# Performance work log

Hardware: AMD Instinct MI355X
Metric: run time of the kernel (lower is better)

Reference implementation:

```python
import jax, jax.numpy as jnp
import numpy as np

D, P, MC = 512, 256, 128   # state dim, obs dim, control dim
H, M, T = 32, 64, 1024     # num filters, Hankel/filter length, horizon
GAMMA = 0.9


def setup_inputs() -> dict:
    rng = np.random.default_rng(0)
    # Stable dynamics: scale spectral radius to 0.95
    A = rng.standard_normal((D, D)).astype(np.float32)
    A *= np.float32(0.95 / np.max(np.abs(np.linalg.eigvals(A))))
    B = (rng.standard_normal((D, MC)) / np.sqrt(D)).astype(np.float32)
    C = (rng.standard_normal((P, D)) / np.sqrt(D)).astype(np.float32)
    # SPD cost matrices
    Q_obs = np.eye(P, dtype=np.float32)
    R = (0.1 * np.eye(MC)).astype(np.float32)
    # LQR-like feedback gain (small, applied to y_obs as in the source)
    K = (0.02 * rng.standard_normal((MC, P))).astype(np.float32)
    # Spectral filters from Hankel matrix: Z_ij = gamma^(i+j+2) * 2/((i+j+2)^3-(i+j+2))
    idx = np.arange(M)
    ij = idx[:, None] + idx[None, :] + 2
    Z = (GAMMA ** ij) * 2.0 / (ij ** 3 - ij)
    w, V = np.linalg.eigh(Z)
    sigma = np.abs(w[-H:])
    phi = V[:, -H:]
    sigma_phi = (sigma ** 0.25)[:, None] * phi.T        # [H, M]
    sigma_phi_M = sigma_phi.astype(np.float32)
    # sum over the inner l-loop of sigma_phi_m (the source sums contributions over l)
    s_m = sigma_phi.sum(axis=1).astype(np.float32)       # [H]
    # Learned controller tensor M_il -> [m_control, H, h, p]
    M_tensor = (0.01 * rng.standard_normal((MC, H, H, P))).astype(np.float32)
    x0 = rng.standard_normal(D).astype(np.float32)
    return {
        "A": jnp.asarray(A), "B": jnp.asarray(B), "C": jnp.asarray(C),
        "Q_obs": jnp.asarray(Q_obs), "R": jnp.asarray(R), "K": jnp.asarray(K),
        "M_tensor": jnp.asarray(M_tensor),
        "sigma_phi_M": jnp.asarray(sigma_phi_M), "s_m": jnp.asarray(s_m),
        "x0": jnp.asarray(x0),
    }


def reference(A, B, C, Q_obs, R, K, M_tensor, sigma_phi_M, s_m, x0):
    h, m = sigma_phi_M.shape          # filters, history window
    mc = B.shape[1]
    p = C.shape[0]

    # CAB[i] = C @ A^i @ B for i = 0..h  (Markov parameters for y_nat)
    def pow_step(Ap, _):
        return Ap @ A, C @ (Ap @ B)
    _, CAB = jax.lax.scan(pow_step, jnp.eye(A.shape[0], dtype=A.dtype), None, length=h + 1)  # [h+1, p, mc]

    # Pre-contract M_tensor with the inner filter weights (sum over j/l):
    # u_pert[c] = sum_{i,k,p'} M2[c,i,p'] * sigma_phi_M[i,k] * y_nat_{t-k}[p']
    M2 = jnp.einsum('cijq,j->ciq', M_tensor, s_m)  # [mc, h, p]

    def step(carry, _):
        x, u_buf, y_buf = carry            # x:[d], u_buf:[h+1,mc] newest-first, y_buf:[m,p] newest-first
        y_obs = C @ x                      # [p]
        # natural observation: strip effect of past controls
        y_nat = y_obs - jnp.einsum('ipc,ic->p', CAB, u_buf)
        y_buf = jnp.concatenate([y_nat[None, :], y_buf[:-1]], axis=0)
        # spectral projection of y_nat history, then contract with learned tensor
        y_proj = sigma_phi_M @ y_buf       # [h, p]
        u_pert = jnp.einsum('ciq,iq->c', M2, y_proj)  # [mc]
        u = -(K @ y_obs) + u_pert
        cost = y_obs @ (Q_obs @ y_obs) + u @ (R @ u)
        u_buf = jnp.concatenate([u[None, :], u_buf[:-1]], axis=0)
        x = A @ x + B @ u
        return (x, u_buf, y_buf), cost

    init = (x0,
            jnp.zeros((h + 1, mc), dtype=x0.dtype),
            jnp.zeros((m, p), dtype=x0.dtype))
    _, costs = jax.lax.scan(step, init, None, length=T)
    return costs  # [T] per-step losses
```

## Files before the change

### kernel.cpp

```cpp
#include <hip/hip_runtime.h>

#define TPB 256
#define MAXJ 48

#define SC_N 128
#define YD0 128
#define YU0 160
#define WD0 167
#define WU0 175
#define DT0 182
#define XP0 198
#define XR0 230
#define U0 246
#define NWG 254
#define NGRP 8
#define GCH 32

__device__ __forceinline__ void cst(float* p, float v) {
  __hip_atomic_store(p, v, __ATOMIC_RELAXED, __HIP_MEMORY_SCOPE_AGENT);
}
__device__ __forceinline__ void cstu(unsigned* p, unsigned v) {
  __hip_atomic_store(p, v, __ATOMIC_RELAXED, __HIP_MEMORY_SCOPE_AGENT);
}
__device__ __forceinline__ unsigned cldu(const unsigned* p) {
  return __hip_atomic_load(p, __ATOMIC_RELAXED, __HIP_MEMORY_SCOPE_AGENT);
}
__device__ __forceinline__ float cld(const float* p) {
  return __hip_atomic_load(p, __ATOMIC_RELAXED, __HIP_MEMORY_SCOPE_AGENT);
}
__device__ __forceinline__ float2 cld2(const float* p) {
  unsigned long long u = __hip_atomic_load(
      reinterpret_cast<const unsigned long long*>(p), __ATOMIC_RELAXED,
      __HIP_MEMORY_SCOPE_AGENT);
  float2 v;
  __builtin_memcpy(&v, &u, 8);
  return v;
}

__device__ __forceinline__ void grid_barrier(unsigned* __restrict__ arr,
                                             unsigned* __restrict__ grp,
                                             int bid, int tid, unsigned phase) {
  asm volatile("s_waitcnt vmcnt(0)" ::: "memory");
  __syncthreads();
  if (tid == 0) cstu(arr + (bid << 5), phase);
  if (bid < NGRP) {
    const int lo = bid * GCH;
    const int n = (NWG - lo < GCH) ? (NWG - lo) : GCH;
    if (tid < n) {
      while (cldu(arr + ((lo + tid) << 5)) < phase) __builtin_amdgcn_s_sleep(1);
    }
    __syncthreads();
    if (tid == 0) cstu(grp + (bid << 5), phase);
  }
  if (tid < NGRP) {
    while (cldu(grp + (tid << 5)) < phase) __builtin_amdgcn_s_sleep(1);
  }
  __atomic_signal_fence(__ATOMIC_SEQ_CST);
  __syncthreads();
}

__device__ void gemm_tile(const float* __restrict__ X, const float* __restrict__ Y,
                          float* __restrict__ Z, int M, int N, int Kd,
                          int mtile, int ntile) {
  __shared__ float Xs[16][65];
  __shared__ float Ys[16][65];
  const int tx = threadIdx.x & 15;
  const int ty = threadIdx.x >> 4;
  const int mbase = mtile * 64;
  const int nbase = ntile * 64;
  float acc[4][4] = {};
  for (int k0 = 0; k0 < Kd; k0 += 16) {
#pragma unroll
    for (int r = 0; r < 4; ++r) {
      int idx = threadIdx.x + 256 * r;
      int mm = idx >> 4, kk = idx & 15;
      int gm = mbase + mm, gk = k0 + kk;
      Xs[kk][mm] = (gm < M && gk < Kd) ? X[(size_t)gm * Kd + gk] : 0.f;
      int nn = idx & 63, k2 = idx >> 6;
      int gn = nbase + nn, gk2 = k0 + k2;
      Ys[k2][nn] = (gk2 < Kd && gn < N) ? Y[(size_t)gk2 * N + gn] : 0.f;
    }
    __syncthreads();
#pragma unroll
    for (int kk = 0; kk < 16; ++kk) {
      float xv[4], yv[4];
#pragma unroll
      for (int a = 0; a < 4; ++a) xv[a] = Xs[kk][ty * 4 + a];
#pragma unroll
      for (int b = 0; b < 4; ++b) yv[b] = Ys[kk][tx * 4 + b];
#pragma unroll
      for (int a = 0; a < 4; ++a)
#pragma unroll
        for (int b = 0; b < 4; ++b) acc[a][b] += xv[a] * yv[b];
    }
    __syncthreads();
  }
#pragma unroll
  for (int a = 0; a < 4; ++a) {
    int gm = mbase + ty * 4 + a;
    if (gm < M) {
#pragma unroll
      for (int b = 0; b < 4; ++b) {
        int gn = nbase + tx * 4 + b;
        if (gn < N) Z[(size_t)gm * N + gn] = acc[a][b];
      }
    }
  }
}

struct JobBatch {
  int n;
  int start[MAXJ + 1];
  int xsel[MAXJ], xoff[MAXJ], ysel[MAXJ], yoff[MAXJ], zoff[MAXJ];
  int M[MAXJ], N[MAXJ], K[MAXJ];
};

__global__ __launch_bounds__(256) void multi_gemm(JobBatch jb,
    const float* __restrict__ A, const float* __restrict__ Bm,
    const float* __restrict__ C, const float* __restrict__ Km,
    float* __restrict__ ws) {
  int b = blockIdx.x;
  int j = 0;
  while (j < jb.n - 1 && b >= jb.start[j + 1]) ++j;
  int rel = b - jb.start[j];
  const float* bases[5] = {ws, A, Bm, C, Km};
  const float* X = bases[jb.xsel[j]] + jb.xoff[j];
  const float* Y = bases[jb.ysel[j]] + jb.yoff[j];
  float* Z = ws + jb.zoff[j];
  int tn = jb.N[j] >> 6;
  gemm_tile(X, Y, Z, jb.M[j], jb.N[j], jb.K[j], rel / tn, rel % tn);
}

__global__ __launch_bounds__(256) void m2_kernel(const float* __restrict__ MT,
    const float* __restrict__ sm, float* __restrict__ M2g) {
  int idx = blockIdx.x * 256 + threadIdx.x;
  if (idx >= 128 * 32 * 256) return;
  int q = idx & 255;
  int ci = idx >> 8;
  const float* base = MT + (size_t)ci * 32 * 256 + q;
  float acc = 0.f;
#pragma unroll
  for (int j = 0; j < 32; ++j) acc += base[j * 256] * sm[j];
  M2g[idx] = acc;
}

__global__ __launch_bounds__(256) void wfir_kernel(const float* __restrict__ M2g,
    const float* __restrict__ Phi, float* __restrict__ W) {
  int idx = blockIdx.x * 256 + threadIdx.x;
  if (idx >= 64 * 32768) return;
  int j = idx >> 15;
  int cq = idx & 32767;
  int c = cq >> 8;
  int q = cq & 255;
  float acc = 0.f;
#pragma unroll
  for (int i = 0; i < 32; ++i)
    acc = fmaf(Phi[(i << 6) | j], M2g[(size_t)(((c << 5) | i) << 8) | q], acc);
  W[idx] = acc;
}

__global__ __launch_bounds__(256) void axpy_acl(const float* __restrict__ A,
    const float* __restrict__ BKC, float* __restrict__ Acl, float* __restrict__ P1) {
  int i = blockIdx.x * 256 + threadIdx.x;
  if (i < 262144) {
    float v = A[i] - BKC[i];
    Acl[i] = v;
    P1[i] = v;
  }
}

__global__ void init_kernel(const float* __restrict__ x0, float* __restrict__ xh,
    float* __restrict__ eh, float* __restrict__ ynh, float* __restrict__ uh0,
    float* __restrict__ dbnd, unsigned* __restrict__ arr,
    unsigned* __restrict__ grp) {
  int i = blockIdx.x * 256 + threadIdx.x;
  int stride = gridDim.x * 256;
  for (int k = i; k < 524288; k += stride) cst(xh + k, 0.f);
  for (int k = i; k < 139264; k += stride) cst(eh + k, 0.f);
  for (int k = i; k < 262144; k += stride) cst(ynh + k, 0.f);
  for (int k = i; k < 8192; k += stride) cst(uh0 + k, 0.f);
  for (int k = i; k < NWG * 32; k += stride) cstu(arr + k, 0u);
  for (int k = i; k < NGRP * 32; k += stride) cstu(grp + k, 0u);
  if (i < 512) cst(dbnd + i, x0[i]);
}

__global__ __launch_bounds__(TPB, 1) void main_kernel(
    const float* __restrict__ B, const float* __restrict__ C,
    const float* __restrict__ x0, const float* __restrict__ Wfir,
    const float* __restrict__ KC, const float* __restrict__ W0C,
    const float* __restrict__ Pp, const float* __restrict__ CAp,
    const float* __restrict__ W0CAp, const float* __restrict__ Rnp,
    const float* __restrict__ AB33p, const float* __restrict__ CAB33p,
    const float* __restrict__ W0CAB33p, const float* __restrict__ A8k,
    float* __restrict__ xh, float* __restrict__ uh0, float* __restrict__ eh,
    float* __restrict__ ynh, float* __restrict__ dbnd,
    unsigned* __restrict__ arr, unsigned* __restrict__ grp) {
  __shared__ float smA[64 * 256];
  __shared__ float smY[8 * 256];
  __shared__ float smV[512];
  __shared__ float smW[8 * 128];
  __shared__ float smVx[8 * 516];
  __shared__ float redsc[4][16];
  const int bid = blockIdx.x;
  const int tid = threadIdx.x;

  if (bid < SC_N) {
    for (int i = tid; i < 16384; i += TPB) {
      int j = i >> 8;
      smA[i] = (j >= 1) ? Wfir[(size_t)j * 32768 + bid * 256 + (i & 255)] : 0.f;
    }
    __syncthreads();
#pragma unroll 1
    for (int ph = 0; ph <= 130; ++ph) {
      if (ph >= 1 && ph < 129) {
        const int Ty = ph * 8 - 8;
        for (int i2 = tid; i2 < 1024; i2 += TPB) {
          float2 v = cld2(ynh + (size_t)Ty * 256 + 2 * i2);
          smY[2 * i2] = v.x;
          smY[2 * i2 + 1] = v.y;
        }
        __syncthreads();
        const int q = tid;
        float yreg[8];
#pragma unroll
        for (int s = 0; s < 8; ++s) yreg[s] = smY[s * 256 + q];
        const int wv = tid >> 6;
        const int lane = tid & 63;
#pragma unroll
        for (int kt = 0; kt < 5; ++kt) {
          const int r0 = 1 + 16 * kt;
          float wreg[23];
#pragma unroll
          for (int i = 0; i < 23; ++i) {
            const int j = r0 - 7 + i;
            wreg[i] = (j >= 1 && j <= 63) ? smA[j * 256 + q] : 0.f;
          }
          float acc[16];
#pragma unroll
          for (int a = 0; a < 16; ++a) acc[a] = 0.f;
#pragma unroll
          for (int a = 0; a < 16; ++a)
#pragma unroll
            for (int s = 0; s < 8; ++s) acc[a] += wreg[a + 7 - s] * yreg[s];
#pragma unroll
          for (int a = 0; a < 16; ++a) {
            float v = acc[a];
            v += __shfl_xor(v, 32);
            v += __shfl_xor(v, 16);
            v += __shfl_xor(v, 8);
            v += __shfl_xor(v, 4);
            v += __shfl_xor(v, 2);
            v += __shfl_xor(v, 1);
            if (lane == 0) redsc[wv][a] = v;
          }
          __syncthreads();
          if (tid < 16) {
            const int r = r0 + tid;
            if (r <= 70) {
              float sum = redsc[0][tid] + redsc[1][tid] + redsc[2][tid] + redsc[3][tid];
              atomicAdd(&eh[(size_t)(Ty + r) * 128 + bid], sum);
            }
          }
          __syncthreads();
        }
      }
      grid_barrier(arr, grp, bid, tid, (unsigned)(ph + 1));
    }
  } else if (bid < YU0) {
    const int r = bid - YD0;
    const int s = r >> 2;
    const int qtr = (r & 3) * 64;
    const int row = qtr + (tid >> 2);
    const int ks = (tid & 3) * 128;
    const float* Mrow = (s == 0) ? C : (CAp + (size_t)(s - 1) * 131072);
    const float4* m4 = (const float4*)(Mrow + (size_t)row * 512 + ks);
#pragma unroll 1
    for (int ph = 0; ph <= 130; ++ph) {
      if (ph < 128) {
        const int T = ph * 8;
        {
          float2 v = cld2(dbnd + (size_t)ph * 512 + 2 * tid);
          smV[2 * tid] = v.x;
          smV[2 * tid + 1] = v.y;
        }
        __syncthreads();
        const float4* v4 = (const float4*)(smV + ks);
        float a = 0.f;
#pragma unroll
        for (int it = 0; it < 32; ++it) {
          float4 mm = m4[it], vv = v4[it];
          a += mm.x * vv.x + mm.y * vv.y + mm.z * vv.z + mm.w * vv.w;
        }
        a += __shfl_down(a, 2);
        a += __shfl_down(a, 1);
        if ((tid & 3) == 0) atomicAdd(&ynh[(size_t)(T + s) * 256 + row], a);
      }
      grid_barrier(arr, grp, bid, tid, (unsigned)(ph + 1));
    }
  } else if (bid < WD0) {
    const int m = bid - YU0;
    const int row = tid;
    const float4* m4 = (const float4*)(CAB33p + (size_t)m * 32768 + (size_t)row * 128);
#pragma unroll 1
    for (int ph = 0; ph <= 130; ++ph) {
      if (ph < 128) {
        const int T = ph * 8;
        for (int i2 = tid; i2 < 512; i2 += TPB) {
          float2 v = cld2(uh0 + (size_t)(64 + T - 33) * 128 + 2 * i2);
          smW[2 * i2] = v.x;
          smW[2 * i2 + 1] = v.y;
        }
        __syncthreads();
        float acc[8];
#pragma unroll
        for (int s = 0; s < 8; ++s) acc[s] = 0.f;
#pragma unroll 4
        for (int it = 0; it < 32; ++it) {
          float4 mm = m4[it];
#pragma unroll
          for (int s = 0; s < 8; ++s) {
            if (s > m) {
              float4 vv = ((const float4*)(smW + (s - m - 1) * 128))[it];
              acc[s] += mm.x * vv.x + mm.y * vv.y + mm.z * vv.z + mm.w * vv.w;
            }
          }
        }
#pragma unroll
        for (int s = 0; s < 8; ++s)
          if (s > m) atomicAdd(&ynh[(size_t)(T + s) * 256 + row], acc[s]);
      }
      grid_barrier(arr, grp, bid, tid, (unsigned)(ph + 1));
    }
  } else if (bid < WU0) {
    const int s = bid - WD0;
    const int row = tid >> 1;
    const int seg = tid & 1;
    const float* Mrow = (s == 0) ? W0C : (W0CAp + (size_t)(s - 1) * 65536);
    const float4* m4 = (const float4*)(Mrow + (size_t)row * 512 + seg * 256);
#pragma unroll 1
    for (int ph = 0; ph <= 130; ++ph) {
      if (ph < 128) {
        const int T = ph * 8;
        {
          float2 v = cld2(dbnd + (size_t)ph * 512 + 2 * tid);
          smV[2 * tid] = v.x;
          smV[2 * tid + 1] = v.y;
        }
        __syncthreads();
        const float4* v4 = (const float4*)(smV + seg * 256);
        float a = 0.f;
#pragma unroll
        for (int it = 0; it < 64; ++it) {
          float4 mm = m4[it], vv = v4[it];
          a += mm.x * vv.x + mm.y * vv.y + mm.z * vv.z + mm.w * vv.w;
        }
        a += __shfl_down(a, 1);
        if (seg == 0) atomicAdd(&eh[(size_t)(T + s) * 128 + row], a);
      }
      grid_barrier(arr, grp, bid, tid, (unsigned)(ph + 1));
    }
  } else if (bid < DT0) {
    const int m = bid - WU0;
    const int row = tid >> 1;
    const int seg = tid & 1;
    const float4* m4 = (const float4*)(W0CAB33p + (size_t)m * 16384 + (size_t)row * 128 + seg * 64);
#pragma unroll 1
    for (int ph = 0; ph <= 130; ++ph) {
      if (ph < 128) {
        const int T = ph * 8;
        for (int i2 = tid; i2 < 512; i2 += TPB) {
          float2 v = cld2(uh0 + (size_t)(64 + T - 33) * 128 + 2 * i2);
          smW[2 * i2] = v.x;
          smW[2 * i2 + 1] = v.y;
        }
        __syncthreads();
        float acc[8];
#pragma unroll
        for (int s = 0; s < 8; ++s) acc[s] = 0.f;
#pragma unroll 4
        for (int it = 0; it < 16; ++it) {
          float4 mm = m4[it];
#pragma unroll
          for (int s = 0; s < 8; ++s) {
            if (s > m) {
              float4 vv = ((const float4*)(smW + (s - m - 1) * 128 + seg * 64))[it];
              acc[s] += mm.x * vv.x + mm.y * vv.y + mm.z * vv.z + mm.w * vv.w;
            }
          }
        }
#pragma unroll
        for (int s = 0; s < 8; ++s) {
          if (s > m) {
            float v = acc[s];
            v += __shfl_down(v, 1);
            if (seg == 0) atomicAdd(&eh[(size_t)(T + s) * 128 + row], v);
          }
        }
      }
      grid_barrier(arr, grp, bid, tid, (unsigned)(ph + 1));
    }
  } else if (bid < XP0) {
    const int g = bid - DT0;
    const int row = g * 32 + (tid >> 3);
    const int l8 = tid & 7;
#pragma unroll 1
    for (int ph = 0; ph <= 130; ++ph) {
      if (ph < 127) {
        const int T = ph * 8;
        {
          float2 v = cld2(dbnd + (size_t)ph * 512 + 2 * tid);
          smV[2 * tid] = v.x;
          smV[2 * tid + 1] = v.y;
        }
        for (int i2 = tid; i2 < 512; i2 += TPB) {
          float2 v = cld2(uh0 + (size_t)(64 + T - 33) * 128 + 2 * i2);
          smW[2 * i2] = v.x;
          smW[2 * i2 + 1] = v.y;
        }
        __syncthreads();
        float a = 0.f;
        {
          const float4* m4 = (const float4*)(A8k + (size_t)row * 512 + l8 * 64);
          const float4* v4 = (const float4*)(smV + l8 * 64);
#pragma unroll
          for (int it = 0; it < 16; ++it) {
            float4 mm = m4[it], vv = v4[it];
            a += mm.x * vv.x + mm.y * vv.y + mm.z * vv.z + mm.w * vv.w;
          }
        }
#pragma unroll
        for (int m = 0; m < 8; ++m) {
          const float4* m4 = (const float4*)(AB33p + (size_t)m * 65536 + (size_t)row * 128 + l8 * 16);
          const float4* v4 = (const float4*)(smW + (7 - m) * 128 + l8 * 16);
#pragma unroll
          for (int it = 0; it < 4; ++it) {
            float4 mm = m4[it], vv = v4[it];
            a += mm.x * vv.x + mm.y * vv.y + mm.z * vv.z + mm.w * vv.w;
          }
        }
        a += __shfl_down(a, 4);
        a += __shfl_down(a, 2);
        a += __shfl_down(a, 1);
        if (l8 == 0) cst(&dbnd[(size_t)(ph + 1) * 512 + row], a);
      }
      grid_barrier(arr, grp, bid, tid, (unsigned)(ph + 1));
    }
  } else if (bid < XR0) {
    const int r = bid - XP0;
    const int s = r >> 2;
    const int qtr = (r & 3) << 7;
    const int row = qtr + (tid >> 1);
    const int seg = tid & 1;
#pragma unroll 1
    for (int ph = 0; ph <= 130; ++ph) {
      if (ph >= 2 && ph < 130) {
        const int Tq = ph * 8 - 16;
        {
          const float* src = (ph == 2) ? x0 : (xh + (size_t)(Tq - 1) * 512);
          float2 v = cld2(src + 2 * tid);
          smV[2 * tid] = v.x;
          smV[2 * tid + 1] = v.y;
        }
        __syncthreads();
        const int pslot = (ph == 2) ? s : (s + 1);
        if (pslot == 0) {
          if (seg == 0) atomicAdd(&xh[(size_t)Tq * 512 + row], smV[row]);
        } else {
          const float4* m4 = (const float4*)(Pp + (size_t)(pslot - 1) * 262144 +
                                             (size_t)row * 512 + seg * 256);
          const float4* v4 = (const float4*)(smV + seg * 256);
          float a = 0.f;
#pragma unroll
          for (int it = 0; it < 64; ++it) {
            float4 mm = m4[it], vv = v4[it];
            a += mm.x * vv.x + mm.y * vv.y + mm.z * vv.z + mm.w * vv.w;
          }
          a += __shfl_down(a, 1);
          if (seg == 0) atomicAdd(&xh[(size_t)(Tq + s) * 512 + row], a);
        }
      }
      grid_barrier(arr, grp, bid, tid, (unsigned)(ph + 1));
    }
  } else if (bid < U0) {
    const int r = bid - XR0;
    const int i = r >> 1;
    const int half = (r & 1) << 8;
    const int row = half + tid;
    const float* Rrow = (i == 0) ? (B + (size_t)row * 128)
                                 : (Rnp + (size_t)(i - 1) * 65536 + (size_t)row * 128);
    const float4* m4 = (const float4*)Rrow;
#pragma unroll 1
    for (int ph = 0; ph <= 130; ++ph) {
      if (ph >= 2 && ph < 130) {
        const int Tq = ph * 8 - 16;
        for (int i2 = tid; i2 < 512; i2 += TPB) {
          int idx = 2 * i2;
          float2 v;
          if (ph == 2 && idx < 128) {
            v.x = 0.f;
            v.y = 0.f;
          } else {
            v = cld2(eh + (size_t)(Tq - 1) * 128 + idx);
          }
          smW[idx] = v.x;
          smW[idx + 1] = v.y;
        }
        __syncthreads();
        float acc[8];
#pragma unroll
        for (int s = 0; s < 8; ++s) acc[s] = 0.f;
#pragma unroll 4
        for (int it = 0; it < 32; ++it) {
          float4 mm = m4[it];
#pragma unroll
          for (int s = 0; s < 8; ++s) {
            if (s >= i) {
              float4 vv = ((const float4*)(smW + (s - i) * 128))[it];
              acc[s] += mm.x * vv.x + mm.y * vv.y + mm.z * vv.z + mm.w * vv.w;
            }
          }
        }
#pragma unroll
        for (int s = 0; s < 8; ++s)
          if (s >= i) atomicAdd(&xh[(size_t)(Tq + s) * 512 + row], acc[s]);
      }
      grid_barrier(arr, grp, bid, tid, (unsigned)(ph + 1));
    }
  } else {
    const int g = bid - U0;
    const int o = tid >> 1;
    const int par = tid & 1;
    const int s = o >> 4;
    const int lr = o & 15;
    const int row = g * 16 + lr;
    const float4* m4 = (const float4*)(KC + (size_t)row * 512 + par * 256);
#pragma unroll 1
    for (int ph = 0; ph <= 130; ++ph) {
      if (ph >= 3) {
        const int Tu = ph * 8 - 24;
        for (int i2 = tid; i2 < 2048; i2 += TPB) {
          int idx = 2 * i2;
          int rr = idx >> 9;
          int cc = idx & 511;
          float2 v = cld2(xh + (size_t)(Tu + rr) * 512 + cc);
          smVx[rr * 516 + cc] = v.x;
          smVx[rr * 516 + cc + 1] = v.y;
        }
        __syncthreads();
        const float4* v4 = (const float4*)(smVx + s * 516 + par * 256);
        float a = 0.f;
#pragma unroll
        for (int it = 0; it < 64; ++it) {
          float4 mm = m4[it], vv = v4[it];
          a += mm.x * vv.x + mm.y * vv.y + mm.z * vv.z + mm.w * vv.w;
        }
        a += __shfl_down(a, 1);
        if (par == 0) {
          float u = cld(&eh[(size_t)(Tu + s) * 128 + row]) - a;
          cst(&uh0[(size_t)(64 + Tu + s) * 128 + row], u);
        }
      }
      grid_barrier(arr, grp, bid, tid, (unsigned)(ph + 1));
    }
  }
}

__global__ __launch_bounds__(256) void cost_kernel(const float* __restrict__ C,
    const float* __restrict__ Q, const float* __restrict__ R,
    const float* __restrict__ xh, const float* __restrict__ uh0,
    float* __restrict__ out) {
  __shared__ float xs[512];
  __shared__ float ys[256];
  __shared__ float us[128];
  __shared__ float redw[4];
  const int t = blockIdx.x;
  const int tid = threadIdx.x;
  {
    float2 v = cld2(xh + (size_t)t * 512 + 2 * tid);
    xs[2 * tid] = v.x;
    xs[2 * tid + 1] = v.y;
  }
  if (tid < 64) {
    float2 v = cld2(uh0 + (size_t)(64 + t) * 128 + 2 * tid);
    us[2 * tid] = v.x;
    us[2 * tid + 1] = v.y;
  }
  __syncthreads();
  {
    const float4* m4 = (const float4*)(C + (size_t)tid * 512);
    const float4* v4 = (const float4*)xs;
    float a = 0.f;
    for (int it = 0; it < 128; ++it) {
      float4 mm = m4[it], vv = v4[it];
      a += mm.x * vv.x + mm.y * vv.y + mm.z * vv.z + mm.w * vv.w;
    }
    ys[tid] = a;
  }
  __syncthreads();
  float acc;
  {
    const float* Qr = Q + (size_t)tid * 256;
    float qy = 0.f;
    for (int k = 0; k < 256; ++k) qy = fmaf(Qr[k], ys[k], qy);
    acc = qy * ys[tid];
  }
  if (tid < 128) {
    const float* Rr = R + (size_t)tid * 128;
    float ru = 0.f;
    for (int k = 0; k < 128; ++k) ru = fmaf(Rr[k], us[k], ru);
    acc += ru * us[tid];
  }
  float v = acc;
  v += __shfl_xor(v, 32);
  v += __shfl_xor(v, 16);
  v += __shfl_xor(v, 8);
  v += __shfl_xor(v, 4);
  v += __shfl_xor(v, 2);
  v += __shfl_xor(v, 1);
  if ((tid & 63) == 0) redw[tid >> 6] = v;
  __syncthreads();
  if (tid == 0) out[t] = redw[0] + redw[1] + redw[2] + redw[3];
}

extern "C" void kernel_launch(void* const* d_in, const int* in_sizes, int n_in,
                              void* d_out, int out_size, void* d_ws, size_t ws_size,
                              hipStream_t stream) {
  (void)in_sizes; (void)n_in; (void)out_size; (void)ws_size;
  const float* A = (const float*)d_in[0];
  const float* B = (const float*)d_in[1];
  const float* C = (const float*)d_in[2];
  const float* Q = (const float*)d_in[3];
  const float* R = (const float*)d_in[4];
  const float* Km = (const float*)d_in[5];
  const float* MT = (const float*)d_in[6];
  const float* Phi = (const float*)d_in[7];
  const float* sm = (const float*)d_in[8];
  const float* x0 = (const float*)d_in[9];

  float* ws = (float*)d_ws;
  const int oWfir = 0;
  const int oKC = 2097152;
  const int oW0C = 2162688;
  const int oAcl = 2228224;
  const int oP = 2490368;
  const int oCA = 4587520;
  const int oW0CA = 5505024;
  const int oRn = 5963776;
  const int oApB = 6422528;
  const int oAB33 = 6946816;
  const int oCAB33 = 7471104;
  const int oW0CAB33 = 7700480;
  const int oA2 = 7815168;
  const int oA4 = 8077312;
  const int oA8 = 8339456;
  const int oA16 = 8601600;
  const int oA32 = 8863744;
  const int oM2 = 9125888;
  const int oBKC = oM2;
  const int oxh = 10174464;
  const int ouh0 = 10698752;
  const int oeh = 10838016;
  const int oynh = 10977280;
  const int odbnd = 11239424;
  const int oarr = 11306496;
  const int ogrp = oarr + NWG * 32;

  float* xh = ws + oxh;
  float* uh0 = ws + ouh0;
  float* eh = ws + oeh;
  float* ynh = ws + oynh;
  float* dbnd = ws + odbnd;
  unsigned* arr = (unsigned*)(ws + oarr);
  unsigned* grp = (unsigned*)(ws + ogrp);

  JobBatch jb;
  jb.n = 0;
  jb.start[0] = 0;
  auto J = [&](int xs_, int xo, int ys_, int yo, int zo, int M, int N, int K) {
    int i = jb.n++;
    jb.xsel[i] = xs_; jb.xoff[i] = xo; jb.ysel[i] = ys_; jb.yoff[i] = yo;
    jb.zoff[i] = zo; jb.M[i] = M; jb.N[i] = N; jb.K[i] = K;
    jb.start[i + 1] = jb.start[i] + (M >> 6) * (N >> 6);
  };
  auto L = [&]() {
    multi_gemm<<<dim3(jb.start[jb.n]), dim3(256), 0, stream>>>(jb, A, B, C, Km, ws);
    jb.n = 0;
    jb.start[0] = 0;
  };

  init_kernel<<<dim3(2048), dim3(256), 0, stream>>>(x0, xh, eh, ynh, uh0, dbnd,
                                                    arr, grp);
  m2_kernel<<<dim3(4096), dim3(256), 0, stream>>>(MT, sm, ws + oM2);
  wfir_kernel<<<dim3(8192), dim3(256), 0, stream>>>(ws + oM2, Phi, ws + oWfir);

  J(4, 0, 3, 0, oKC, 128, 512, 256);
  J(1, 0, 1, 0, oA2, 512, 512, 512);
  J(1, 0, 2, 0, oApB, 512, 128, 512);
  J(3, 0, 1, 0, oCA, 256, 512, 512);
  L();
  J(2, 0, 0, oKC, oBKC, 512, 512, 128);
  J(0, oA2, 0, oA2, oA4, 512, 512, 512);
  J(0, oCA, 1, 0, oCA + 131072, 256, 512, 512);
  J(1, 0, 0, oApB, oApB + 65536, 512, 128, 512);
  J(0, oWfir, 3, 0, oW0C, 128, 512, 256);
  L();
  axpy_acl<<<dim3(1024), dim3(256), 0, stream>>>(A, ws + oBKC, ws + oAcl, ws + oP);
  J(0, oA4, 0, oA4, oA8, 512, 512, 512);
  J(0, oP, 0, oP, oP + 262144, 512, 512, 512);
  J(0, oCA, 0, oA2, oCA + 2 * 131072, 256, 512, 512);
  J(0, oCA + 131072, 0, oA2, oCA + 3 * 131072, 256, 512, 512);
  J(0, oW0C, 1, 0, oW0CA, 128, 512, 512);
  J(0, oW0C, 0, oA2, oW0CA + 65536, 128, 512, 512);
  J(0, oA2, 0, oApB, oApB + 2 * 65536, 512, 128, 512);
  J(0, oA2, 0, oApB + 65536, oApB + 3 * 65536, 512, 128, 512);
  L();
  J(0, oA8, 0, oA8, oA16, 512, 512, 512);
  J(0, oP, 0, oP + 262144, oP + 2 * 262144, 512, 512, 512);
  J(0, oP + 262144, 0, oP + 262144, oP + 3 * 262144, 512, 512, 512);
  for (int i = 1; i <= 3; ++i)
    J(0, oCA + (i - 1) * 131072, 0, oA4, oCA + (i + 3) * 131072, 256, 512, 512);
  for (int i = 1; i <= 2; ++i)
    J(0, oW0CA + (i - 1) * 65536, 0, oA2, oW0CA + (i + 1) * 65536, 128, 512, 512);
  for (int k = 1; k <= 4; ++k)
    J(0, oA4, 0, oApB + (k - 1) * 65536, oApB + (k + 3) * 65536, 512, 128, 512);
  J(0, oP, 2, 0, oRn, 512, 128, 512);
  J(0, oP + 262144, 2, 0, oRn + 65536, 512, 128, 512);
  L();
  J(0, oA16, 0, oA16, oA32, 512, 512, 512);
  for (int i = 1; i <= 4; ++i)
    J(0, oP + (i - 1) * 262144, 0, oP + 3 * 262144, oP + (i + 3) * 262144, 512, 512, 512);
  for (int i = 1; i <= 3; ++i)
    J(0, oW0CA + (i - 1) * 65536, 0, oA4, oW0CA + (i + 3) * 65536, 128, 512, 512);
  J(0, oP + 2 * 262144, 2, 0, oRn + 2 * 65536, 512, 128, 512);
  J(0, oP + 3 * 262144, 2, 0, oRn + 3 * 65536, 512, 128, 512);
  L();
  for (int m = 0; m <= 7; ++m)
    J(0, oA32, 0, oApB + m * 65536, oAB33 + m * 65536, 512, 128, 512);
  for (int i = 5; i <= 7; ++i)
    J(0, oP + (i - 1) * 262144, 2, 0, oRn + (i - 1) * 65536, 512, 128, 512);
  L();
  for (int m = 0; m <= 6; ++m)
    J(3, 0, 0, oAB33 + m * 65536, oCAB33 + m * 32768, 256, 128, 512);
  for (int m = 0; m <= 6; ++m)
    J(0, oW0C, 0, oAB33 + m * 65536, oW0CAB33 + m * 16384, 128, 128, 512);
  L();

  main_kernel<<<dim3(NWG), dim3(TPB), 0, stream>>>(
      B, C, x0, ws + oWfir, ws + oKC, ws + oW0C, ws + oP, ws + oCA,
      ws + oW0CA, ws + oRn, ws + oAB33, ws + oCAB33, ws + oW0CAB33,
      ws + oA8, xh, uh0, eh, ynh, dbnd, arr, grp);

  cost_kernel<<<dim3(1024), dim3(256), 0, stream>>>(C, Q, R, xh, uh0,
                                                    (float*)d_out);
}
```

Measured before the change: 3.358 ms.

## Use three-level tree grid barrier and register-ring FIR with direct stores

Replaces the two-level grid barrier with a tree barrier: groups of 16 workgroups are gathered by blocks in the DT stage, a single root aggregates them, and per-group broadcast flags release waiters. Each workgroup then polls one flag instead of eight. The spectral FIR blocks now keep a 72-entry register ring of y history and compute only the 8 new outputs per phase, writing them with plain stores to a new efir buffer. This replaces the old banded recomputation that used atomics into eh. Consumers now sum eh and efir, which costs an extra load and a large register footprint, and the barrier gains one more level of latency.

```diff
diff --git a/kernel.cpp b/kernel.cpp
--- a/kernel.cpp
+++ b/kernel.cpp
@@ -13,8 +13,6 @@
 #define XR0 230
 #define U0 246
 #define NWG 254
-#define NGRP 8
-#define GCH 32
 
 __device__ __forceinline__ void cst(float* p, float v) {
   __hip_atomic_store(p, v, __ATOMIC_RELAXED, __HIP_MEMORY_SCOPE_AGENT);
@@ -37,23 +35,33 @@
   return v;
 }
 
-__device__ __forceinline__ void grid_barrier(unsigned* __restrict__ arr,
-                                             unsigned* __restrict__ grp,
-                                             int bid, int tid, unsigned phase) {
+__device__ __forceinline__ void tree_barrier(unsigned* __restrict__ arr,
+                                             unsigned* __restrict__ gl,
+                                             unsigned* __restrict__ bc,
+                                             int bid, int tid, unsigned v) {
   asm volatile("s_waitcnt vmcnt(0)" ::: "memory");
   __syncthreads();
-  if (tid == 0) cstu(arr + (bid << 5), phase);
-  if (bid < NGRP) {
-    const int lo = bid * GCH;
-    const int n = (NWG - lo < GCH) ? (NWG - lo) : GCH;
+  if (tid == 0) cstu(arr + (bid << 5), v);
+  if (bid >= DT0 && bid < DT0 + 16) {
+    const int g = bid - DT0;
+    const int lo = g << 4;
+    const int n = (NWG - lo < 16) ? (NWG - lo) : 16;
     if (tid < n) {
-      while (cldu(arr + ((lo + tid) << 5)) < phase) __builtin_amdgcn_s_sleep(1);
+      while (cldu(arr + ((lo + tid) << 5)) < v) __builtin_amdgcn_s_sleep(2);
     }
     __syncthreads();
-    if (tid == 0) cstu(grp + (bid << 5), phase);
-  }
-  if (tid < NGRP) {
-    while (cldu(grp + (tid << 5)) < phase) __builtin_amdgcn_s_sleep(1);
+    if (tid == 0) cstu(gl + (g << 5), v);
+  }
+  if (bid == DT0) {
+    if (tid < 16) {
+      while (cldu(gl + (tid << 5)) < v) __builtin_amdgcn_s_sleep(2);
+    }
+    __syncthreads();
+    if (tid < 16) cstu(bc + (tid << 5), v);
+  }
+  if (tid == 0) {
+    const int g = bid >> 4;
+    while (cldu(bc + (g << 5)) < v) __builtin_amdgcn_s_sleep(2);
   }
   __atomic_signal_fence(__ATOMIC_SEQ_CST);
   __syncthreads();
@@ -172,7 +180,7 @@
 __global__ void init_kernel(const float* __restrict__ x0, float* __restrict__ xh,
     float* __restrict__ eh, float* __restrict__ ynh, float* __restrict__ uh0,
     float* __restrict__ dbnd, unsigned* __restrict__ arr,
-    unsigned* __restrict__ grp) {
+    unsigned* __restrict__ gl, unsigned* __restrict__ bc) {
   int i = blockIdx.x * 256 + threadIdx.x;
   int stride = gridDim.x * 256;
   for (int k = i; k < 524288; k += stride) cst(xh + k, 0.f);
@@ -180,7 +188,10 @@
   for (int k = i; k < 262144; k += stride) cst(ynh + k, 0.f);
   for (int k = i; k < 8192; k += stride) cst(uh0 + k, 0.f);
   for (int k = i; k < NWG * 32; k += stride) cstu(arr + k, 0u);
-  for (int k = i; k < NGRP * 32; k += stride) cstu(grp + k, 0u);
+  for (int k = i; k < 16 * 32; k += stride) {
+    cstu(gl + k, 0u);
+    cstu(bc + k, 0u);
+  }
   if (i < 512) cst(dbnd + i, x0[i]);
 }
 
@@ -193,10 +204,10 @@
     const float* __restrict__ AB33p, const float* __restrict__ CAB33p,
     const float* __restrict__ W0CAB33p, const float* __restrict__ A8k,
     float* __restrict__ xh, float* __restrict__ uh0, float* __restrict__ eh,
-    float* __restrict__ ynh, float* __restrict__ dbnd,
-    unsigned* __restrict__ arr, unsigned* __restrict__ grp) {
+    float* __restrict__ efir, float* __restrict__ ynh, float* __restrict__ dbnd,
+    unsigned* __restrict__ arr, unsigned* __restrict__ gl,
+    unsigned* __restrict__ bc) {
   __shared__ float smA[64 * 256];
-  __shared__ float smY[8 * 256];
   __shared__ float smV[512];
   __shared__ float smW[8 * 128];
   __shared__ float smVx[8 * 516];
@@ -210,61 +221,47 @@
       smA[i] = (j >= 1) ? Wfir[(size_t)j * 32768 + bid * 256 + (i & 255)] : 0.f;
     }
     __syncthreads();
+    float ring[72];
+#pragma unroll
+    for (int k = 0; k < 72; ++k) ring[k] = 0.f;
+    const int wv = tid >> 6;
+    const int lane = tid & 63;
 #pragma unroll 1
     for (int ph = 0; ph <= 130; ++ph) {
       if (ph >= 1 && ph < 129) {
         const int Ty = ph * 8 - 8;
-        for (int i2 = tid; i2 < 1024; i2 += TPB) {
-          float2 v = cld2(ynh + (size_t)Ty * 256 + 2 * i2);
-          smY[2 * i2] = v.x;
-          smY[2 * i2 + 1] = v.y;
-        }
-        __syncthreads();
-        const int q = tid;
-        float yreg[8];
-#pragma unroll
-        for (int s = 0; s < 8; ++s) yreg[s] = smY[s * 256 + q];
-        const int wv = tid >> 6;
-        const int lane = tid & 63;
-#pragma unroll
-        for (int kt = 0; kt < 5; ++kt) {
-          const int r0 = 1 + 16 * kt;
-          float wreg[23];
-#pragma unroll
-          for (int i = 0; i < 23; ++i) {
-            const int j = r0 - 7 + i;
-            wreg[i] = (j >= 1 && j <= 63) ? smA[j * 256 + q] : 0.f;
-          }
-          float acc[16];
-#pragma unroll
-          for (int a = 0; a < 16; ++a) acc[a] = 0.f;
-#pragma unroll
-          for (int a = 0; a < 16; ++a)
-#pragma unroll
-            for (int s = 0; s < 8; ++s) acc[a] += wreg[a + 7 - s] * yreg[s];
-#pragma unroll
-          for (int a = 0; a < 16; ++a) {
-            float v = acc[a];
-            v += __shfl_xor(v, 32);
-            v += __shfl_xor(v, 16);
-            v += __shfl_xor(v, 8);
-            v += __shfl_xor(v, 4);
-            v += __shfl_xor(v, 2);
-            v += __shfl_xor(v, 1);
-            if (lane == 0) redsc[wv][a] = v;
-          }
-          __syncthreads();
-          if (tid < 16) {
-            const int r = r0 + tid;
-            if (r <= 70) {
-              float sum = redsc[0][tid] + redsc[1][tid] + redsc[2][tid] + redsc[3][tid];
-              atomicAdd(&eh[(size_t)(Ty + r) * 128 + bid], sum);
-            }
-          }
-          __syncthreads();
-        }
-      }
-      grid_barrier(arr, grp, bid, tid, (unsigned)(ph + 1));
+#pragma unroll
+        for (int k = 0; k < 64; ++k) ring[k] = ring[k + 8];
+#pragma unroll
+        for (int s = 0; s < 8; ++s)
+          ring[64 + s] = cld(ynh + (size_t)(Ty + s) * 256 + tid);
+        float acc[8];
+#pragma unroll
+        for (int s = 0; s < 8; ++s) acc[s] = 0.f;
+#pragma unroll
+        for (int m = 1; m <= 63; ++m) {
+          float w = smA[m * 256 + tid];
+#pragma unroll
+          for (int s = 0; s < 8; ++s) acc[s] = fmaf(w, ring[64 + s - m], acc[s]);
+        }
+#pragma unroll
+        for (int s = 0; s < 8; ++s) {
+          float v = acc[s];
+          v += __shfl_xor(v, 32);
+          v += __shfl_xor(v, 16);
+          v += __shfl_xor(v, 8);
+          v += __shfl_xor(v, 4);
+          v += __shfl_xor(v, 2);
+          v += __shfl_xor(v, 1);
+          if (lane == 0) redsc[wv][s] = v;
+        }
+        __syncthreads();
+        if (tid < 8) {
+          float sum = redsc[0][tid] + redsc[1][tid] + redsc[2][tid] + redsc[3][tid];
+          cst(efir + (size_t)(Ty + tid) * 128 + bid, sum);
+        }
+      }
+      tree_barrier(arr, gl, bc, bid, tid, (unsigned)(ph + 1));
     }
   } else if (bid < YU0) {
     const int r = bid - YD0;
@@ -295,7 +292,7 @@
         a += __shfl_down(a, 1);
         if ((tid & 3) == 0) atomicAdd(&ynh[(size_t)(T + s) * 256 + row], a);
       }
-      grid_barrier(arr, grp, bid, tid, (unsigned)(ph + 1));
+      tree_barrier(arr, gl, bc, bid, tid, (unsigned)(ph + 1));
     }
   } else if (bid < WD0) {
     const int m = bid - YU0;
@@ -329,7 +326,7 @@
         for (int s = 0; s < 8; ++s)
           if (s > m) atomicAdd(&ynh[(size_t)(T + s) * 256 + row], acc[s]);
       }
-      grid_barrier(arr, grp, bid, tid, (unsigned)(ph + 1));
+      tree_barrier(arr, gl, bc, bid, tid, (unsigned)(ph + 1));
     }
   } else if (bid < WU0) {
     const int s = bid - WD0;
@@ -357,7 +354,7 @@
         a += __shfl_down(a, 1);
         if (seg == 0) atomicAdd(&eh[(size_t)(T + s) * 128 + row], a);
       }
-      grid_barrier(arr, grp, bid, tid, (unsigned)(ph + 1));
+      tree_barrier(arr, gl, bc, bid, tid, (unsigned)(ph + 1));
     }
   } else if (bid < DT0) {
     const int m = bid - WU0;
@@ -397,7 +394,7 @@
           }
         }
       }
-      grid_barrier(arr, grp, bid, tid, (unsigned)(ph + 1));
+      tree_barrier(arr, gl, bc, bid, tid, (unsigned)(ph + 1));
     }
   } else if (bid < XP0) {
     const int g = bid - DT0;
@@ -443,7 +440,7 @@
         a += __shfl_down(a, 1);
         if (l8 == 0) cst(&dbnd[(size_t)(ph + 1) * 512 + row], a);
       }
-      grid_barrier(arr, grp, bid, tid, (unsigned)(ph + 1));
+      tree_barrier(arr, gl, bc, bid, tid, (unsigned)(ph + 1));
     }
   } else if (bid < XR0) {
     const int r = bid - XP0;
@@ -479,7 +476,7 @@
           if (seg == 0) atomicAdd(&xh[(size_t)(Tq + s) * 512 + row], a);
         }
       }
-      grid_barrier(arr, grp, bid, tid, (unsigned)(ph + 1));
+      tree_barrier(arr, gl, bc, bid, tid, (unsigned)(ph + 1));
     }
   } else if (bid < U0) {
     const int r = bid - XR0;
@@ -500,7 +497,10 @@
             v.x = 0.f;
             v.y = 0.f;
           } else {
-            v = cld2(eh + (size_t)(Tq - 1) * 128 + idx);
+            float2 a2 = cld2(eh + (size_t)(Tq - 1) * 128 + idx);
+            float2 b2 = cld2(efir + (size_t)(Tq - 1) * 128 + idx);
+            v.x = a2.x + b2.x;
+            v.y = a2.y + b2.y;
           }
           smW[idx] = v.x;
           smW[idx + 1] = v.y;
@@ -524,7 +524,7 @@
         for (int s = 0; s < 8; ++s)
           if (s >= i) atomicAdd(&xh[(size_t)(Tq + s) * 512 + row], acc[s]);
       }
-      grid_barrier(arr, grp, bid, tid, (unsigned)(ph + 1));
+      tree_barrier(arr, gl, bc, bid, tid, (unsigned)(ph + 1));
     }
   } else {
     const int g = bid - U0;
@@ -556,11 +556,12 @@
         }
         a += __shfl_down(a, 1);
         if (par == 0) {
-          float u = cld(&eh[(size_t)(Tu + s) * 128 + row]) - a;
+          float u = cld(&eh[(size_t)(Tu + s) * 128 + row]) +
+                    cld(&efir[(size_t)(Tu + s) * 128 + row]) - a;
           cst(&uh0[(size_t)(64 + Tu + s) * 128 + row], u);
         }
       }
-      grid_barrier(arr, grp, bid, tid, (unsigned)(ph + 1));
+      tree_barrier(arr, gl, bc, bid, tid, (unsigned)(ph + 1));
     }
   }
 }
@@ -662,16 +663,20 @@
   const int oeh = 10838016;
   const int oynh = 10977280;
   const int odbnd = 11239424;
-  const int oarr = 11306496;
-  const int ogrp = oarr + NWG * 32;
+  const int oefir = 11306496;
+  const int oarr = 11437568;
+  const int ogl = oarr + NWG * 32;
+  const int obc = ogl + 512;
 
   float* xh = ws + oxh;
   float* uh0 = ws + ouh0;
   float* eh = ws + oeh;
   float* ynh = ws + oynh;
   float* dbnd = ws + odbnd;
+  float* efir = ws + oefir;
   unsigned* arr = (unsigned*)(ws + oarr);
-  unsigned* grp = (unsigned*)(ws + ogrp);
+  unsigned* gl = (unsigned*)(ws + ogl);
+  unsigned* bc = (unsigned*)(ws + obc);
 
   JobBatch jb;
   jb.n = 0;
@@ -689,7 +694,7 @@
   };
 
   init_kernel<<<dim3(2048), dim3(256), 0, stream>>>(x0, xh, eh, ynh, uh0, dbnd,
-                                                    arr, grp);
+                                                    arr, gl, bc);
   m2_kernel<<<dim3(4096), dim3(256), 0, stream>>>(MT, sm, ws + oM2);
   wfir_kernel<<<dim3(8192), dim3(256), 0, stream>>>(ws + oM2, Phi, ws + oWfir);
 
@@ -748,7 +753,7 @@
   main_kernel<<<dim3(NWG), dim3(TPB), 0, stream>>>(
       B, C, x0, ws + oWfir, ws + oKC, ws + oW0C, ws + oP, ws + oCA,
       ws + oW0CA, ws + oRn, ws + oAB33, ws + oCAB33, ws + oW0CAB33,
-      ws + oA8, xh, uh0, eh, ynh, dbnd, arr, grp);
+      ws + oA8, xh, uh0, eh, efir, ynh, dbnd, arr, gl, bc);
 
   cost_kernel<<<dim3(1024), dim3(256), 0, stream>>>(C, Q, R, xh, uh0,
                                                     (float*)d_out);
```

New measurement: 3.131 ms. 6.8% less time.
